# Optimization experiments

Measured on AMD Instinct MI355X. Metric: run time of the kernel, lower is better.

Reference implementation:

```python
import jax, jax.numpy as jnp
import numpy as np

H = 16      # num_heads
D = 64      # head_dim
SCALE = (2 * D) ** -0.5


def setup_inputs() -> dict:
    key = jax.random.key(0)
    k1, k2, k3, k4, k5 = jax.random.split(key, 5)
    tokens = jax.random.normal(k1, (4, 2048, 1024), dtype=jnp.float32)
    sen = jax.random.normal(k2, (4, 1, 1024), dtype=jnp.float32)
    W1 = jax.random.normal(k3, (1024, 3072), dtype=jnp.float32) * (1024 ** -0.5)
    W2 = jax.random.normal(k4, (1024, 2048), dtype=jnp.float32) * (1024 ** -0.5)
    mask = jax.random.randint(k5, (4, 2048), 0, 2, dtype=jnp.int32)
    return {"tokens": tokens, "sen": sen, "W1": W1, "W2": W2, "mask": mask}


def _split_heads(t):
    # [b, n, h*d] -> [b, h, n, d]
    b, n, _ = t.shape
    return t.reshape(b, n, H, D).transpose(0, 2, 1, 3)


def reference(tokens, sen, W1, W2, mask):
    b, n, _ = tokens.shape
    # token-stream qkv: [b, n, 3*h*d]
    q1, k1, v1 = (_split_heads(t) for t in jnp.split(tokens @ W1, 3, axis=-1))
    # sentence-stream qk: sen has seq len 1 -> [b, h, 1, d]
    q2, k2 = (_split_heads(t) for t in jnp.split(sen @ W2, 2, axis=-1))
    # dual-source scores: [b,h,n,n] + broadcast [b,h,1,1]
    dots = SCALE * (jnp.einsum('bhnd,bhmd->bhnm', q1, k1)
                    + jnp.einsum('bhnd,bhmd->bhnm', q2, k2))
    m = mask[:, None, None, :].astype(dots.dtype)
    dots = dots - 10000.0 * (1.0 - m)
    attn = jax.nn.softmax(dots, axis=-1)
    out = jnp.einsum('bhnm,bhmd->bhnd', attn, v1)
    return out.transpose(0, 2, 1, 3).reshape(b, n, H * D)
```

## Files before the change

kernel.cpp:

```cpp
#include <hip/hip_runtime.h>
#include <cstdint>


typedef __bf16 bf16x8 __attribute__((ext_vector_type(8)));
typedef __bf16 bf16x4 __attribute__((ext_vector_type(4)));
typedef float  f32x4  __attribute__((ext_vector_type(4)));
typedef float  f32x16 __attribute__((ext_vector_type(16)));
typedef unsigned int u32x4 __attribute__((ext_vector_type(4)));

#define MFMA16(a,b,c) __builtin_amdgcn_mfma_f32_16x16x32_bf16(a,b,c,0,0,0)
#define MFMA32(a,b,c) __builtin_amdgcn_mfma_f32_32x32x16_bf16(a,b,c,0,0,0)

static __device__ __forceinline__ float exp2_raw(float x) {
    float r; asm("v_exp_f32 %0, %1" : "=v"(r) : "v"(x)); return r;
}
static __device__ __forceinline__ uint32_t pkbf16(float a, float b) {
    uint32_t r; asm("v_cvt_pk_bf16_f32 %0, %1, %2" : "=v"(r) : "v"(a), "v"(b)); return r;
}
static __device__ __forceinline__ void lds_fence() {
    asm volatile("s_waitcnt lgkmcnt(0)" ::: "memory");
    __builtin_amdgcn_sched_barrier(0);
}
static __device__ __forceinline__ f32x16 zero16() {
    f32x16 z;
#pragma unroll
    for (int i = 0; i < 16; ++i) z[i] = 0.f;
    return z;
}
static __device__ __forceinline__ bf16x8 zero8() {
    return __builtin_bit_cast(bf16x8, (u32x4){0u, 0u, 0u, 0u});
}

#define GLLDS(src, dst)                                                        \
    __builtin_amdgcn_global_load_lds(                                          \
        (const __attribute__((address_space(1))) void*)(src),                  \
        (__attribute__((address_space(3))) void*)(dst), 16, 0, 0)

static constexpr float QSCALE = 0.12751879523486166f;

__global__ __launch_bounds__(256) void k_cvt_tok(const float* __restrict__ in,
                                                 __bf16* __restrict__ out) {
    int i = (blockIdx.x * 256 + threadIdx.x) * 4;
    float4 v = *(const float4*)&in[i];
    bf16x4 o = {(__bf16)v.x, (__bf16)v.y, (__bf16)v.z, (__bf16)v.w};
    *(bf16x4*)&out[i] = o;
}

__global__ __launch_bounds__(256) void k_w1t(const float* __restrict__ W1,
                                             __bf16* __restrict__ W1T) {
    __shared__ float t[32][33];
    int bx = blockIdx.x % 96, by = blockIdx.x / 96;
    int r0 = by * 32, c0 = bx * 32;
    int tr = threadIdx.x >> 3, tc = (threadIdx.x & 7) * 4;
    float4 v = *(const float4*)&W1[(size_t)(r0 + tr) * 3072 + c0 + tc];
    t[tr][tc + 0] = v.x; t[tr][tc + 1] = v.y; t[tr][tc + 2] = v.z; t[tr][tc + 3] = v.w;
    __syncthreads();
    bf16x4 o = {(__bf16)t[tc + 0][tr], (__bf16)t[tc + 1][tr],
                (__bf16)t[tc + 2][tr], (__bf16)t[tc + 3][tr]};
    *(bf16x4*)&W1T[(size_t)(c0 + tr) * 1024 + r0 + tc] = o;
}

__global__ __launch_bounds__(256) void k_mask(const int* __restrict__ m,
                                              __bf16* __restrict__ fl,
                                              __bf16* __restrict__ flp) {
    int i = blockIdx.x * 256 + threadIdx.x;
    fl[i] = (__bf16)(float)m[i];
    int s6 = i & 63;
    int kp = ((s6 >> 2) & 1) * 32 + ((s6 >> 4) & 3) * 8 + ((s6 >> 3) & 1) * 4 + (s6 & 3);
    flp[i] = (__bf16)(float)m[(i & ~63) | kp];
}

__global__ __launch_bounds__(256) void k_gemm_qkv(const __bf16* __restrict__ A,
                                                  const __bf16* __restrict__ BT,
                                                  const __bf16* __restrict__ FLAG,
                                                  __bf16* __restrict__ Q,
                                                  __bf16* __restrict__ K,
                                                  __bf16* __restrict__ VT) {
    __shared__ __align__(16) char gsm[32768];
    const int tid = threadIdx.x;
    const int bid = blockIdx.x;
    const int sw = (bid & 7) * 192 + (bid >> 3);
    const int tm = sw / 24, tn = sw % 24;
    const int m0 = tm * 128, n0 = tn * 128;
    const int l = tid & 63, wv = tid >> 6;
    const int l15 = l & 15, l4 = l >> 4;
    const int wr = wv >> 1, wc = wv & 1;

    const char* Ab = (const char*)A;
    const char* Bb = (const char*)BT;
    const size_t aoff = (size_t)(m0 + wv * 32 + (l >> 2)) * 2048 + (l & 3) * 16;
    const size_t boff = (size_t)(n0 + wv * 32 + (l >> 2)) * 2048 + (l & 3) * 16;

    f32x4 acc[4][4];
#pragma unroll
    for (int i = 0; i < 4; ++i)
#pragma unroll
        for (int j = 0; j < 4; ++j) acc[i][j] = (f32x4){0.f, 0.f, 0.f, 0.f};

    auto STAGE = [&](int nb, int kt) {
        char* ab = gsm + nb * 16384 + wv * 2048;
        char* bb = ab + 8192;
#pragma unroll
        for (int i = 0; i < 2; ++i) {
            GLLDS(Ab + aoff + (size_t)i * 32768 + (size_t)kt * 64, ab + i * 1024);
            GLLDS(Bb + boff + (size_t)i * 32768 + (size_t)kt * 64, bb + i * 1024);
        }
    };
    STAGE(0, 0);

    for (int kt = 0; kt < 32; ++kt) {
        const int cur = kt & 1;
        __syncthreads();
        if (kt < 31) STAGE(cur ^ 1, kt + 1);
        const char* As = gsm + cur * 16384;
        const char* Bs = As + 8192;

        bf16x8 af[4], bb[4];
#pragma unroll
        for (int mi = 0; mi < 4; ++mi)
            af[mi] = *(const bf16x8*)(As + (wr * 64 + mi * 16 + l15) * 64 + l4 * 16);
#pragma unroll
        for (int ni = 0; ni < 4; ++ni)
            bb[ni] = *(const bf16x8*)(Bs + (wc * 64 + ni * 16 + l15) * 64 + l4 * 16);
#pragma unroll
        for (int mi = 0; mi < 4; ++mi)
#pragma unroll
            for (int ni = 0; ni < 4; ++ni)
                acc[mi][ni] = MFMA16(af[mi], bb[ni], acc[mi][ni]);
    }

#pragma unroll
    for (int mi = 0; mi < 4; ++mi) {
        const int rowb = m0 + wr * 64 + mi * 16 + l4 * 4;
        const int b = rowb >> 11, n = rowb & 2047;
#pragma unroll
        for (int ni = 0; ni < 4; ++ni) {
            const int col = n0 + wc * 64 + ni * 16 + l15;
            const int str = col >> 10, cc = col & 1023;
            const int h = cc >> 6, d = cc & 63;
            const int bh = b * 16 + h;
            if (str == 2) {
                const bf16x4 fv = *(const bf16x4*)&FLAG[b * 2048 + n];
                bf16x4 pv = {(__bf16)(acc[mi][ni][0] * (float)fv[0]),
                             (__bf16)(acc[mi][ni][1] * (float)fv[1]),
                             (__bf16)(acc[mi][ni][2] * (float)fv[2]),
                             (__bf16)(acc[mi][ni][3] * (float)fv[3])};
                const int k6 = n & 63;
                const int nsl = (n & ~63) | (((k6 >> 3) & 3) << 4) |
                                (((k6 >> 2) & 1) << 3) | ((k6 >> 5) << 2);
                *(bf16x4*)&VT[((size_t)bh * 64 + d) * 2048 + nsl] = pv;
            } else if (str == 0) {
#pragma unroll
                for (int r = 0; r < 4; ++r)
                    Q[((size_t)bh * 2048 + n + r) * 64 + d] = (__bf16)(acc[mi][ni][r] * QSCALE);
            } else {
#pragma unroll
                for (int r = 0; r < 4; ++r)
                    K[((size_t)bh * 2048 + n + r) * 64 + d] = (__bf16)acc[mi][ni][r];
            }
        }
    }
}

__global__ __launch_bounds__(256, 2) void k_attn(const __bf16* __restrict__ Q,
                                                 const __bf16* __restrict__ K,
                                                 const __bf16* __restrict__ VT,
                                                 const __bf16* __restrict__ FLAGP,
                                                 float* __restrict__ out) {
    __shared__ __align__(16) char smem[33280];
    const int tid = threadIdx.x;
    const int bid = blockIdx.x;
    const int swz = (bid & 7) * 64 + (bid >> 3);
    const int bh = swz >> 3, qt = swz & 7;
    const int b = bh >> 4, h = bh & 15;
    const int wv = tid >> 6, l = tid & 63, l31 = l & 31, hi = l >> 5;

    const char* Kg = (const char*)K + (size_t)bh * 2048 * 128;
    const char* Vg = (const char*)VT + (size_t)bh * 64 * 4096;
    const __bf16* Fg = FLAGP + b * 2048;

    const __bf16* qp = Q + ((size_t)bh * 2048 + qt * 256 + wv * 64 + l31) * 64;
    bf16x8 qf0[4], qf1[4];
#pragma unroll
    for (int m = 0; m < 4; ++m) {
        qf0[m] = *(const bf16x8*)(qp + m * 16 + hi * 8);
        qf1[m] = *(const bf16x8*)(qp + 32 * 64 + m * 16 + hi * 8);
    }

    f32x16 o00 = zero16(), o01 = zero16(), o10 = zero16(), o11 = zero16();
    f32x16 fa0 = zero16(), fa1 = zero16();
    float mr0 = -1e30f, mr1 = -1e30f;

    auto STAGE = [&](int nb, int t) {
        char* base = smem + nb * 16384;
#pragma unroll
        for (int i = 0; i < 2; ++i) {
            const int blk = wv + i * 4;
            const int mc = blk >> 1, rb = blk & 1;
            const int row = rb * 32 + (l >> 1);
            GLLDS(Kg + (size_t)(t * 64 + row) * 128 + mc * 32 + (l & 1) * 16,
                  base + blk * 1024);
            GLLDS(Vg + (size_t)row * 4096 + t * 128 + mc * 32 + (l & 1) * 16,
                  base + 8192 + blk * 1024);
        }
    };
    STAGE(0, 0);

    for (int t = 0; t < 32; ++t) {
        const int cur = t & 1;
        __syncthreads();
        if (t < 31) STAGE(cur ^ 1, t + 1);
        const char* Ks = smem + cur * 16384;
        const char* Vs = Ks + 8192;

        bf16x8 kf0[4], kf1[4];
#pragma unroll
        for (int m = 0; m < 4; ++m) {
            kf0[m] = *(const bf16x8*)(Ks + m * 2048 + l31 * 32 + hi * 16);
            kf1[m] = *(const bf16x8*)(Ks + m * 2048 + (32 + l31) * 32 + hi * 16);
        }

        f32x16 s0 = zero16(), s1 = zero16();
#pragma unroll
        for (int m = 0; m < 4; ++m) s0 = MFMA32(kf0[m], qf0[m], s0);
#pragma unroll
        for (int m = 0; m < 4; ++m) s1 = MFMA32(kf1[m], qf0[m], s1);
        {
            float mx = fmaxf(s0[0], s1[0]);
#pragma unroll
            for (int i = 1; i < 16; ++i) mx = fmaxf(mx, fmaxf(s0[i], s1[i]));
            mx = fmaxf(mx, __shfl_xor(mx, 32, 64));
            if (!__all(mx <= mr0 + 8.0f)) {
                float mn = fmaxf(mr0, mx);
                float al = exp2_raw(mr0 - mn);
                o00 *= al; o01 *= al; fa0 *= al; mr0 = mn;
            }
        }
        u32x4 pk0[4];
#pragma unroll
        for (int m = 0; m < 4; ++m) {
            pk0[m].x = pkbf16(exp2_raw(s0[4 * m] - mr0), exp2_raw(s0[4 * m + 1] - mr0));
            pk0[m].y = pkbf16(exp2_raw(s0[4 * m + 2] - mr0), exp2_raw(s0[4 * m + 3] - mr0));
            pk0[m].z = pkbf16(exp2_raw(s1[4 * m] - mr0), exp2_raw(s1[4 * m + 1] - mr0));
            pk0[m].w = pkbf16(exp2_raw(s1[4 * m + 2] - mr0), exp2_raw(s1[4 * m + 3] - mr0));
        }

        bf16x8 ff[4];
#pragma unroll
        for (int m = 0; m < 4; ++m) ff[m] = zero8();
        if (l31 == 0) {
#pragma unroll
            for (int m = 0; m < 4; ++m)
                ff[m] = *(const bf16x8*)(Fg + t * 64 + m * 16 + hi * 8);
        }

        s0 = zero16(); s1 = zero16();
#pragma unroll
        for (int m = 0; m < 4; ++m) s0 = MFMA32(kf0[m], qf1[m], s0);
#pragma unroll
        for (int m = 0; m < 4; ++m) s1 = MFMA32(kf1[m], qf1[m], s1);
        {
            float mx = fmaxf(s0[0], s1[0]);
#pragma unroll
            for (int i = 1; i < 16; ++i) mx = fmaxf(mx, fmaxf(s0[i], s1[i]));
            mx = fmaxf(mx, __shfl_xor(mx, 32, 64));
            if (!__all(mx <= mr1 + 8.0f)) {
                float mn = fmaxf(mr1, mx);
                float al = exp2_raw(mr1 - mn);
                o10 *= al; o11 *= al; fa1 *= al; mr1 = mn;
            }
        }
        u32x4 pk1[4];
#pragma unroll
        for (int m = 0; m < 4; ++m) {
            pk1[m].x = pkbf16(exp2_raw(s0[4 * m] - mr1), exp2_raw(s0[4 * m + 1] - mr1));
            pk1[m].y = pkbf16(exp2_raw(s0[4 * m + 2] - mr1), exp2_raw(s0[4 * m + 3] - mr1));
            pk1[m].z = pkbf16(exp2_raw(s1[4 * m] - mr1), exp2_raw(s1[4 * m + 1] - mr1));
            pk1[m].w = pkbf16(exp2_raw(s1[4 * m + 2] - mr1), exp2_raw(s1[4 * m + 3] - mr1));
        }

#pragma unroll
        for (int m = 0; m < 4; ++m) {
            bf16x8 vf0 = *(const bf16x8*)(Vs + m * 2048 + l31 * 32 + hi * 16);
            bf16x8 vf1 = *(const bf16x8*)(Vs + m * 2048 + (32 + l31) * 32 + hi * 16);
            bf16x8 p0 = __builtin_bit_cast(bf16x8, pk0[m]);
            bf16x8 p1 = __builtin_bit_cast(bf16x8, pk1[m]);
            o00 = MFMA32(vf0, p0, o00);
            o01 = MFMA32(vf1, p0, o01);
            o10 = MFMA32(vf0, p1, o10);
            o11 = MFMA32(vf1, p1, o11);
            fa0 = MFMA32(ff[m], p0, fa0);
            fa1 = MFMA32(ff[m], p1, fa1);
        }
    }

    __syncthreads();
    float* osm = (float*)smem + wv * 2080;
    const size_t obase = ((size_t)b * 2048 + qt * 256 + wv * 64) * 1024 + h * 64 + l;
    {
        const float inv = 1.0f / __shfl(fa0[0], l31, 64);
#pragma unroll
        for (int r = 0; r < 16; ++r) {
            const int d = (r & 3) + 8 * (r >> 2) + 4 * hi;
            osm[l31 * 65 + d] = o00[r] * inv;
            osm[l31 * 65 + d + 32] = o01[r] * inv;
        }
        lds_fence();
#pragma unroll
        for (int qi = 0; qi < 32; ++qi)
            out[obase + (size_t)qi * 1024] = osm[qi * 65 + l];
        lds_fence();
    }
    {
        const float inv = 1.0f / __shfl(fa1[0], l31, 64);
#pragma unroll
        for (int r = 0; r < 16; ++r) {
            const int d = (r & 3) + 8 * (r >> 2) + 4 * hi;
            osm[l31 * 65 + d] = o10[r] * inv;
            osm[l31 * 65 + d + 32] = o11[r] * inv;
        }
        lds_fence();
#pragma unroll
        for (int qi = 0; qi < 32; ++qi)
            out[obase + (size_t)(32 + qi) * 1024] = osm[qi * 65 + l];
    }
}

extern "C" void kernel_launch(void* const* d_in, const int* in_sizes, int n_in,
                              void* d_out, int out_size, void* d_ws, size_t ws_size,
                              hipStream_t stream) {
    const float* tokens = (const float*)d_in[0];
    const float* W1 = (const float*)d_in[2];
    const int* mask = (const int*)d_in[4];
    float* out = (float*)d_out;

    char* w = (char*)d_ws;
    __bf16* tokbf = (__bf16*)(w + 0);
    __bf16* w1t   = (__bf16*)(w + 16777216);
    __bf16* qarr  = (__bf16*)(w + 23068672);
    __bf16* karr  = (__bf16*)(w + 39845888);
    __bf16* vtar  = (__bf16*)(w + 56623104);
    __bf16* flagb = (__bf16*)(w + 73400320);
    __bf16* flagp = (__bf16*)(w + 73416704);

    k_cvt_tok<<<8192, 256, 0, stream>>>(tokens, tokbf);
    k_w1t<<<3072, 256, 0, stream>>>(W1, w1t);
    k_mask<<<32, 256, 0, stream>>>(mask, flagb, flagp);
    k_gemm_qkv<<<1536, 256, 0, stream>>>(tokbf, w1t, flagb, qarr, karr, vtar);
    k_attn<<<512, 256, 0, stream>>>(qarr, karr, vtar, flagp, out);
}
```

Baseline: 264.8 us.

## Stage Q/K GEMM epilogue through LDS, fuse mask kernel, add MFMA priority hints

Q and K output tiles from the QKV GEMM are now written to shared memory and then stored to global memory as 16-byte rows, replacing scattered 2-byte stores. The separate mask-conversion kernel is folded into the token-conversion kernel, which removes one launch. The attention kernel also raises wave priority around its MFMA blocks to favour matrix-core issue. The price is an extra LDS round-trip with barriers and a slightly larger shared-memory buffer in the GEMM.

```diff
diff --git a/kernel.cpp b/kernel.cpp
--- a/kernel.cpp
+++ b/kernel.cpp
@@ -39,11 +39,21 @@
 static constexpr float QSCALE = 0.12751879523486166f;
 
 __global__ __launch_bounds__(256) void k_cvt_tok(const float* __restrict__ in,
-                                                 __bf16* __restrict__ out) {
-    int i = (blockIdx.x * 256 + threadIdx.x) * 4;
+                                                 const int* __restrict__ m,
+                                                 __bf16* __restrict__ out,
+                                                 __bf16* __restrict__ fl,
+                                                 __bf16* __restrict__ flp) {
+    int gi = blockIdx.x * 256 + threadIdx.x;
+    int i = gi * 4;
     float4 v = *(const float4*)&in[i];
     bf16x4 o = {(__bf16)v.x, (__bf16)v.y, (__bf16)v.z, (__bf16)v.w};
     *(bf16x4*)&out[i] = o;
+    if (gi < 8192) {
+        fl[gi] = (__bf16)(float)m[gi];
+        int s6 = gi & 63;
+        int kp = ((s6 >> 2) & 1) * 32 + ((s6 >> 4) & 3) * 8 + ((s6 >> 3) & 1) * 4 + (s6 & 3);
+        flp[gi] = (__bf16)(float)m[(gi & ~63) | kp];
+    }
 }
 
 __global__ __launch_bounds__(256) void k_w1t(const float* __restrict__ W1,
@@ -60,23 +70,13 @@
     *(bf16x4*)&W1T[(size_t)(c0 + tr) * 1024 + r0 + tc] = o;
 }
 
-__global__ __launch_bounds__(256) void k_mask(const int* __restrict__ m,
-                                              __bf16* __restrict__ fl,
-                                              __bf16* __restrict__ flp) {
-    int i = blockIdx.x * 256 + threadIdx.x;
-    fl[i] = (__bf16)(float)m[i];
-    int s6 = i & 63;
-    int kp = ((s6 >> 2) & 1) * 32 + ((s6 >> 4) & 3) * 8 + ((s6 >> 3) & 1) * 4 + (s6 & 3);
-    flp[i] = (__bf16)(float)m[(i & ~63) | kp];
-}
-
 __global__ __launch_bounds__(256) void k_gemm_qkv(const __bf16* __restrict__ A,
                                                   const __bf16* __restrict__ BT,
                                                   const __bf16* __restrict__ FLAG,
                                                   __bf16* __restrict__ Q,
                                                   __bf16* __restrict__ K,
                                                   __bf16* __restrict__ VT) {
-    __shared__ __align__(16) char gsm[32768];
+    __shared__ __align__(16) char gsm[34816];
     const int tid = threadIdx.x;
     const int bid = blockIdx.x;
     const int sw = (bid & 7) * 192 + (bid >> 3);
@@ -129,18 +129,43 @@
                 acc[mi][ni] = MFMA16(af[mi], bb[ni], acc[mi][ni]);
     }
 
-#pragma unroll
-    for (int mi = 0; mi < 4; ++mi) {
-        const int rowb = m0 + wr * 64 + mi * 16 + l4 * 4;
-        const int b = rowb >> 11, n = rowb & 2047;
-#pragma unroll
-        for (int ni = 0; ni < 4; ++ni) {
-            const int col = n0 + wc * 64 + ni * 16 + l15;
-            const int str = col >> 10, cc = col & 1023;
-            const int h = cc >> 6, d = cc & 63;
-            const int bh = b * 16 + h;
-            if (str == 2) {
-                const bf16x4 fv = *(const bf16x4*)&FLAG[b * 2048 + n];
+    __syncthreads();
+
+    if (tn < 16) {
+        const float scl = (tn < 8) ? QSCALE : 1.0f;
+        char* csm = gsm;
+#pragma unroll
+        for (int mi = 0; mi < 4; ++mi) {
+            const int row = wr * 64 + mi * 16 + l4 * 4;
+#pragma unroll
+            for (int ni = 0; ni < 4; ++ni) {
+                const int col = wc * 64 + ni * 16 + l15;
+#pragma unroll
+                for (int r = 0; r < 4; ++r)
+                    *(__bf16*)(csm + (row + r) * 272 + col * 2) =
+                        (__bf16)(acc[mi][ni][r] * scl);
+            }
+        }
+        __syncthreads();
+        const int row = tid >> 1, hh = tid & 1;
+        const int rowg = m0 + row;
+        const int b = rowg >> 11, n = rowg & 2047;
+        const int h = ((n0 & 1023) >> 6) + hh;
+        __bf16* dst = ((tn < 8) ? Q : K) + ((size_t)(b * 16 + h) * 2048 + n) * 64;
+#pragma unroll
+        for (int j = 0; j < 8; ++j)
+            *(uint4*)(dst + j * 8) = *(const uint4*)(csm + row * 272 + hh * 128 + j * 16);
+    } else {
+#pragma unroll
+        for (int mi = 0; mi < 4; ++mi) {
+            const int rowb = m0 + wr * 64 + mi * 16 + l4 * 4;
+            const int b = rowb >> 11, n = rowb & 2047;
+            const bf16x4 fv = *(const bf16x4*)&FLAG[b * 2048 + n];
+#pragma unroll
+            for (int ni = 0; ni < 4; ++ni) {
+                const int col = n0 + wc * 64 + ni * 16 + l15;
+                const int cc = col & 1023;
+                const int h = cc >> 6, d = cc & 63;
                 bf16x4 pv = {(__bf16)(acc[mi][ni][0] * (float)fv[0]),
                              (__bf16)(acc[mi][ni][1] * (float)fv[1]),
                              (__bf16)(acc[mi][ni][2] * (float)fv[2]),
@@ -148,15 +173,7 @@
                 const int k6 = n & 63;
                 const int nsl = (n & ~63) | (((k6 >> 3) & 3) << 4) |
                                 (((k6 >> 2) & 1) << 3) | ((k6 >> 5) << 2);
-                *(bf16x4*)&VT[((size_t)bh * 64 + d) * 2048 + nsl] = pv;
-            } else if (str == 0) {
-#pragma unroll
-                for (int r = 0; r < 4; ++r)
-                    Q[((size_t)bh * 2048 + n + r) * 64 + d] = (__bf16)(acc[mi][ni][r] * QSCALE);
-            } else {
-#pragma unroll
-                for (int r = 0; r < 4; ++r)
-                    K[((size_t)bh * 2048 + n + r) * 64 + d] = (__bf16)acc[mi][ni][r];
+                *(bf16x4*)&VT[((size_t)(b * 16 + h) * 64 + d) * 2048 + nsl] = pv;
             }
         }
     }
@@ -221,10 +238,12 @@
         }
 
         f32x16 s0 = zero16(), s1 = zero16();
+        __builtin_amdgcn_s_setprio(1);
 #pragma unroll
         for (int m = 0; m < 4; ++m) s0 = MFMA32(kf0[m], qf0[m], s0);
 #pragma unroll
         for (int m = 0; m < 4; ++m) s1 = MFMA32(kf1[m], qf0[m], s1);
+        __builtin_amdgcn_s_setprio(0);
         {
             float mx = fmaxf(s0[0], s1[0]);
 #pragma unroll
@@ -255,10 +274,12 @@
         }
 
         s0 = zero16(); s1 = zero16();
+        __builtin_amdgcn_s_setprio(1);
 #pragma unroll
         for (int m = 0; m < 4; ++m) s0 = MFMA32(kf0[m], qf1[m], s0);
 #pragma unroll
         for (int m = 0; m < 4; ++m) s1 = MFMA32(kf1[m], qf1[m], s1);
+        __builtin_amdgcn_s_setprio(0);
         {
             float mx = fmaxf(s0[0], s1[0]);
 #pragma unroll
@@ -279,6 +300,7 @@
             pk1[m].w = pkbf16(exp2_raw(s1[4 * m + 2] - mr1), exp2_raw(s1[4 * m + 3] - mr1));
         }
 
+        __builtin_amdgcn_s_setprio(1);
 #pragma unroll
         for (int m = 0; m < 4; ++m) {
             bf16x8 vf0 = *(const bf16x8*)(Vs + m * 2048 + l31 * 32 + hi * 16);
@@ -292,6 +314,7 @@
             fa0 = MFMA32(ff[m], p0, fa0);
             fa1 = MFMA32(ff[m], p1, fa1);
         }
+        __builtin_amdgcn_s_setprio(0);
     }
 
     __syncthreads();
@@ -343,9 +366,8 @@
     __bf16* flagb = (__bf16*)(w + 73400320);
     __bf16* flagp = (__bf16*)(w + 73416704);
 
-    k_cvt_tok<<<8192, 256, 0, stream>>>(tokens, tokbf);
+    k_cvt_tok<<<8192, 256, 0, stream>>>(tokens, mask, tokbf, flagb, flagp);
     k_w1t<<<3072, 256, 0, stream>>>(W1, w1t);
-    k_mask<<<32, 256, 0, stream>>>(mask, flagb, flagp);
     k_gemm_qkv<<<1536, 256, 0, stream>>>(tokbf, w1t, flagb, qarr, karr, vtar);
     k_attn<<<512, 256, 0, stream>>>(qarr, karr, vtar, flagp, out);
 }
```

Result: no change. 269.4 us (+1.7%).
